# Performance work log

Hardware: AMD Instinct MI355X
Metric: run time of the kernel (lower is better)

## Reference

```python
import jax, jax.numpy as jnp
import numpy as np

MODES = 32
WIDTH = 64


def crelu(z):
    # split-complex ReLU (torch.relu is undefined on complex; this is the standard fix)
    return jax.nn.relu(z.real) + 1j * jax.nn.relu(z.imag)


def _linear_params(key, fan_in, fan_out):
    k1, k2 = jax.random.split(key)
    s = 1.0 / np.sqrt(fan_in)
    W = jax.random.uniform(k1, (fan_out, fan_in), minval=-s, maxval=s, dtype=jnp.float32)
    b = jax.random.uniform(k2, (fan_out,), minval=-s, maxval=s, dtype=jnp.float32)
    return W, b


def setup_inputs() -> dict:
    key = jax.random.key(0)
    ks = jax.random.split(key, 8)
    B, G = 32768, 512
    H0, H1, H2 = 1024, 512, 64  # hidden_layers; H2 == WIDTH
    FD = 128                    # field_dim
    geometry_input = jax.random.normal(ks[0], (B, G), dtype=jnp.float32)
    W_in, b_in = _linear_params(ks[1], G, H0)
    W_h1, b_h1 = _linear_params(ks[2], H0, H1)
    W_h2, b_h2 = _linear_params(ks[3], H1, H2)
    w0 = jax.random.normal(ks[4], (MODES, WIDTH), dtype=jnp.float32)
    w1 = jax.random.normal(ks[5], (MODES, WIDTH), dtype=jnp.float32)
    lin1_W, lin1_b = _linear_params(ks[6], WIDTH, WIDTH)
    k7a, k7b = jax.random.split(ks[7])
    lin2_W, lin2_b = _linear_params(k7a, WIDTH, WIDTH)
    W_out, b_out = _linear_params(k7b, H2, FD)
    return dict(geometry_input=geometry_input, W_in=W_in, b_in=b_in,
                W_h1=W_h1, b_h1=b_h1, W_h2=W_h2, b_h2=b_h2,
                w0=w0, w1=w1, lin1_W=lin1_W, lin1_b=lin1_b,
                lin2_W=lin2_W, lin2_b=lin2_b, W_out=W_out, b_out=b_out)


def reference(geometry_input, W_in, b_in, W_h1, b_h1, W_h2, b_h2,
              w0, w1, lin1_W, lin1_b, lin2_W, lin2_b, W_out, b_out):
    # MLP encoder: [B, G] -> [B, 64]
    x = jax.nn.relu(geometry_input @ W_in.T + b_in)
    x = jax.nn.relu(x @ W_h1.T + b_h1)
    x = jax.nn.relu(x @ W_h2.T + b_h2)
    # FNO block
    xh = jnp.fft.fftn(x)  # fftn over ALL axes, as in torch code -> complex64 [B, 64]
    phase = jnp.exp(1j * 2.0 * jnp.pi * jnp.arange(MODES) / MODES).astype(jnp.complex64)
    y = xh[:, None, :] * w0  # per-mode lift: [B, MODES, WIDTH]
    y = crelu(y)
    y = y * phase[None, :, None]  # diagonal L mode-multiply
    y = jnp.einsum('bmw,mw->bw', y, w1.astype(y.dtype))  # collapse modes -> [B, WIDTH]
    y = crelu(y @ lin1_W.T + lin1_b)  # real weights on complex acts
    y = y @ lin2_W.T + lin2_b
    y = jnp.fft.ifftn(y)  # [B, 64] complex
    out = y @ W_out.T + b_out  # [B, field_dim] complex
    return out
```

## Files before the change

### kernel.cpp

```cpp
#include <hip/hip_runtime.h>
#include <hip/hip_bf16.h>


#define PI2F 6.28318530717958647692f

typedef __attribute__((ext_vector_type(8))) short short8;
typedef __attribute__((ext_vector_type(4))) float f32x4;

__device__ __forceinline__ unsigned short f2bf(float f) {
  unsigned int u = __float_as_uint(f);
  u += 0x7fff + ((u >> 16) & 1);
  return (unsigned short)(u >> 16);
}
__device__ __forceinline__ unsigned int pack_bf16x2(float a, float b) {
  return (unsigned int)f2bf(a) | ((unsigned int)f2bf(b) << 16);
}

__device__ __forceinline__ void gl2lds16(const void* gptr, const void* lptr) {
  __builtin_amdgcn_global_load_lds(
      (const __attribute__((address_space(1))) unsigned int*)(unsigned long long)gptr,
      (__attribute__((address_space(3))) unsigned int*)(unsigned int)(unsigned long long)lptr,
      16, 0, 0);
}

__global__ __launch_bounds__(256) void f32_to_bf16_k(
    const float* __restrict__ src, unsigned short* __restrict__ dst, int n4)
{
  int i = blockIdx.x * 256 + threadIdx.x;
  if (i < n4) {
    float4 v = ((const float4*)src)[i];
    uint2 p;
    p.x = pack_bf16x2(v.x, v.y);
    p.y = pack_bf16x2(v.z, v.w);
    ((uint2*)dst)[i] = p;
  }
}

template<int BM, int BN, int WM, int WN, typename OUT>
__global__ __launch_bounds__(256) void gemm_async(
    const unsigned short* __restrict__ A, const unsigned short* __restrict__ Bw,
    const float* __restrict__ bias, OUT* __restrict__ C,
    int M, int N, int K)
{
  constexpr int BK = 64;
  __shared__ __align__(16) unsigned short lA[BM * BK];
  __shared__ __align__(16) unsigned short lB[BN * BK];
  const int tid = threadIdx.x;
  const int lane = tid & 63;
  const int wv = tid >> 6;
  const int q = lane >> 4, lr = lane & 15;
  const int x7 = lr & 7;
  constexpr int WN_CNT = BN / WN;
  const int wm = (wv / WN_CNT) * WM;
  const int wn = (wv % WN_CNT) * WN;
  const size_t m0 = (size_t)blockIdx.x * BM;
  const size_t n0 = (size_t)blockIdx.y * BN;
  constexpr int MI = WM / 16, NI = WN / 16;
  f32x4 acc[MI][NI] = {};
  constexpr int A_INSTR = BM * BK / 512;
  constexpr int B_INSTR = BN * BK / 512;
  constexpr int A_PW = A_INSTR / 4, B_PW = B_INSTR / 4;
  (void)M;

  for (int k0 = 0; k0 < K; k0 += BK) {
    __syncthreads();
    #pragma unroll
    for (int s = 0; s < A_PW; ++s) {
      int instr = wv * A_PW + s;
      int pc = instr * 64 + lane;
      int row = pc >> 3, col = pc & 7;
      int lc = col ^ (row & 7);
      gl2lds16(A + (m0 + row) * K + k0 + lc * 8, lA + instr * 512);
    }
    #pragma unroll
    for (int s = 0; s < B_PW; ++s) {
      int instr = wv * B_PW + s;
      int pc = instr * 64 + lane;
      int row = pc >> 3, col = pc & 7;
      int lc = col ^ (row & 7);
      gl2lds16(Bw + (n0 + row) * K + k0 + lc * 8, lB + instr * 512);
    }
    __syncthreads();
    #pragma unroll
    for (int t = 0; t < 2; ++t) {
      short8 af[MI], bfr[NI];
      #pragma unroll
      for (int i = 0; i < MI; ++i) {
        int r = wm + i * 16 + lr;
        af[i] = *(const short8*)(lA + r * 64 + (((t << 2) | q) ^ x7) * 8);
      }
      #pragma unroll
      for (int j = 0; j < NI; ++j) {
        int r = wn + j * 16 + lr;
        bfr[j] = *(const short8*)(lB + r * 64 + (((t << 2) | q) ^ x7) * 8);
      }
      #pragma unroll
      for (int i = 0; i < MI; ++i)
        #pragma unroll
        for (int j = 0; j < NI; ++j)
          acc[i][j] = __builtin_amdgcn_mfma_f32_16x16x32_bf16(af[i], bfr[j], acc[i][j], 0, 0, 0);
    }
  }
  #pragma unroll
  for (int i = 0; i < MI; ++i)
    #pragma unroll
    for (int j = 0; j < NI; ++j) {
      size_t col = n0 + wn + j * 16 + lr;
      float bv = bias[col];
      #pragma unroll
      for (int r = 0; r < 4; ++r) {
        size_t row = m0 + wm + i * 16 + q * 4 + r;
        float v = acc[i][j][r] + bv;
        v = v > 0.f ? v : 0.f;
        if (sizeof(OUT) == 2) ((unsigned short*)C)[row * N + col] = f2bf(v);
        else                  ((float*)C)[row * N + col] = v;
      }
    }
}

__global__ __launch_bounds__(256) void precompute(
    const float* __restrict__ w0, const float* __restrict__ w1,
    const float* __restrict__ l2W, const float* __restrict__ l2b,
    float2* __restrict__ Ap, float2* __restrict__ Am,
    float2* __restrict__ Q, float2* __restrict__ b2c)
{
  const int t = threadIdx.x;
  const int blk = blockIdx.x;
  if (blk == 0) {
    if (t < 64) {
      float apx = 0, apy = 0, amx = 0, amy = 0;
      for (int m = 0; m < 32; ++m) {
        float s0 = w0[m * 64 + t];
        float cf = w1[m * 64 + t] * s0;
        float sn, cs; sincosf(PI2F * (float)m / 32.f, &sn, &cs);
        if (s0 > 0.f)      { apx += cs * cf; apy += sn * cf; }
        else if (s0 < 0.f) { amx += cs * cf; amy += sn * cf; }
      }
      Ap[t] = make_float2(apx, apy);
      Am[t] = make_float2(amx, amy);
      float bx = 0, by = 0;
      for (int k = 0; k < 64; ++k) {
        float sn, cs; sincosf(PI2F * (float)((t * k) & 63) / 64.f, &sn, &cs);
        float lb = l2b[k] * (1.f / 64.f);
        bx += cs * lb; by += sn * lb;
      }
      b2c[t] = make_float2(bx, by);
    }
  } else {
    int e = (blk - 1) * 256 + t;
    int j = e >> 6, w = e & 63;
    float qx = 0, qy = 0;
    for (int k = 0; k < 64; ++k) {
      float sn, cs; sincosf(PI2F * (float)((j * k) & 63) / 64.f, &sn, &cs);
      float lw = l2W[k * 64 + w] * (1.f / 64.f);
      qx += cs * lw; qy += sn * lw;
    }
    Q[j * 64 + w] = make_float2(qx, qy);
  }
}

__global__ __launch_bounds__(256) void dft64_rows(
    const float* __restrict__ x3, float2* __restrict__ xh1)
{
  __shared__ float xt[64][64];
  __shared__ float2 tw[64];
  const int t = threadIdx.x;
  const size_t b0 = (size_t)blockIdx.x * 64;
  for (int it = 0; it < 16; ++it) {
    int idx = it * 256 + t;
    int r = idx >> 6, w = idx & 63;
    xt[r][w] = x3[(b0 + r) * 64 + w];
  }
  if (t < 64) {
    float sn, cs; sincosf(-PI2F * (float)t / 64.f, &sn, &cs);
    tw[t] = make_float2(cs, sn);
  }
  __syncthreads();
  const int k = t & 63, rg = t >> 6;
  float2 acc[16] = {};
  #pragma unroll 1
  for (int w = 0; w < 64; ++w) {
    float2 tv = tw[(k * w) & 63];
    #pragma unroll
    for (int r = 0; r < 16; ++r) {
      float xv = xt[rg * 16 + r][w];
      acc[r].x += xv * tv.x;
      acc[r].y += xv * tv.y;
    }
  }
  for (int r = 0; r < 16; ++r)
    xh1[(b0 + rg * 16 + r) * 64 + k] = acc[r];
}

template<int SIGN>
__global__ __launch_bounds__(256) void fft_stage1(
    const float2* __restrict__ Xin, float2* __restrict__ T)
{
  __shared__ float2 tile[128 * 33];
  __shared__ float2 tw16s[16];
  const int blk = blockIdx.x;
  const int b2 = blk >> 1, wh = (blk & 1) * 32;
  const int t = threadIdx.x;
  for (int it = 0; it < 16; ++it) {
    int idx = it * 256 + t;
    int b1 = idx >> 5, wi = idx & 31;
    tile[b1 * 33 + wi] = Xin[((size_t)(b1 * 256 + b2)) * 64 + wh + wi];
  }
  if (t < 16) {
    float sn, cs; sincosf(SIGN * PI2F * (float)t / 16.f, &sn, &cs);
    tw16s[t] = make_float2(cs, sn);
  }
  __syncthreads();
  const int p = t >> 1, n2a = p >> 4, k1pa = p & 15, w0 = (t & 1) * 16;
  float2 ya[16] = {};
  #pragma unroll 1
  for (int n1 = 0; n1 < 16; ++n1) {
    float2 tv = tw16s[(n1 * k1pa) & 15];
    const float2* row = &tile[(8 * n1 + n2a) * 33 + w0];
    #pragma unroll
    for (int w = 0; w < 16; ++w) {
      float2 d = row[w];
      ya[w].x += d.x * tv.x - d.y * tv.y;
      ya[w].y += d.x * tv.y + d.y * tv.x;
    }
  }
  {
    float sn, cs; sincosf(SIGN * PI2F * (float)(n2a * k1pa) / 128.f, &sn, &cs);
    #pragma unroll
    for (int w = 0; w < 16; ++w) {
      float2 a = ya[w];
      ya[w] = make_float2(a.x * cs - a.y * sn, a.x * sn + a.y * cs);
    }
  }
  __syncthreads();
  {
    float2* yrow = &tile[(n2a * 16 + k1pa) * 33 + w0];
    #pragma unroll
    for (int w = 0; w < 16; ++w) yrow[w] = ya[w];
  }
  __syncthreads();
  const int wB = t & 31, qB = t >> 5;
  float sstep, cstep;
  sincosf(SIGN * PI2F * (float)(16 * b2) / 32768.f, &sstep, &cstep);
  #pragma unroll 1
  for (int h = 0; h < 2; ++h) {
    const int k1p = qB + 8 * h;
    float2 acc[8] = {};
    #pragma unroll 1
    for (int n2 = 0; n2 < 8; ++n2) {
      float2 d = tile[(n2 * 16 + k1p) * 33 + wB];
      #pragma unroll
      for (int k2p = 0; k2p < 8; ++k2p) {
        float2 tv = tw16s[(2 * n2 * k2p) & 15];
        acc[k2p].x += d.x * tv.x - d.y * tv.y;
        acc[k2p].y += d.x * tv.y + d.y * tv.x;
      }
    }
    float sb, cb;
    sincosf(SIGN * PI2F * (float)(b2 * k1p) / 32768.f, &sb, &cb);
    float2 rot = make_float2(cb, sb);
    #pragma unroll
    for (int k2p = 0; k2p < 8; ++k2p) {
      int k1 = k1p + 16 * k2p;
      float2 a = acc[k2p];
      float2 o = make_float2(a.x * rot.x - a.y * rot.y,
                             a.x * rot.y + a.y * rot.x);
      T[((size_t)k1 * 256 + b2) * 64 + wh + wB] = o;
      float nrx = rot.x * cstep - rot.y * sstep;
      rot.y = rot.x * sstep + rot.y * cstep;
      rot.x = nrx;
    }
  }
}

template<int SIGN, bool SCALE>
__global__ __launch_bounds__(256) void fft_stage2(
    const float2* __restrict__ T, float2* __restrict__ X)
{
  __shared__ float2 tile[256 * 17];
  __shared__ float2 tw16s[16];
  const int blk = blockIdx.x;
  const int k1 = blk >> 2, wq = (blk & 3) * 16;
  const int t = threadIdx.x;
  for (int it = 0; it < 16; ++it) {
    int idx = it * 256 + t;
    int r2 = idx >> 4, wi = idx & 15;
    tile[r2 * 17 + wi] = T[((size_t)k1 * 256 + r2) * 64 + wq + wi];
  }
  if (t < 16) {
    float sn, cs; sincosf(SIGN * PI2F * (float)t / 16.f, &sn, &cs);
    tw16s[t] = make_float2(cs, sn);
  }
  __syncthreads();
  const int n2a = t >> 4, k1pa = t & 15;
  float2 ya[16] = {};
  #pragma unroll 1
  for (int n1 = 0; n1 < 16; ++n1) {
    float2 tv = tw16s[(n1 * k1pa) & 15];
    const float2* row = &tile[(16 * n1 + n2a) * 17];
    #pragma unroll
    for (int w = 0; w < 16; ++w) {
      float2 d = row[w];
      ya[w].x += d.x * tv.x - d.y * tv.y;
      ya[w].y += d.x * tv.y + d.y * tv.x;
    }
  }
  {
    float sn, cs; sincosf(SIGN * PI2F * (float)(n2a * k1pa) / 256.f, &sn, &cs);
    #pragma unroll
    for (int w = 0; w < 16; ++w) {
      float2 a = ya[w];
      ya[w] = make_float2(a.x * cs - a.y * sn, a.x * sn + a.y * cs);
    }
  }
  __syncthreads();
  {
    float2* yrow = &tile[(n2a * 16 + k1pa) * 17];
    #pragma unroll
    for (int w = 0; w < 16; ++w) yrow[w] = ya[w];
  }
  __syncthreads();
  const int k1pb = t >> 4, wB = t & 15;
  float2 acc[16] = {};
  #pragma unroll 1
  for (int n2 = 0; n2 < 16; ++n2) {
    float2 d = tile[(n2 * 16 + k1pb) * 17 + wB];
    #pragma unroll
    for (int k2p = 0; k2p < 16; ++k2p) {
      float2 tv = tw16s[(n2 * k2p) & 15];
      acc[k2p].x += d.x * tv.x - d.y * tv.y;
      acc[k2p].y += d.x * tv.y + d.y * tv.x;
    }
  }
  const float sc = SCALE ? (1.f / 32768.f) : 1.f;
  #pragma unroll
  for (int k2p = 0; k2p < 16; ++k2p) {
    int k2 = k1pb + 16 * k2p;
    size_t row = (size_t)(k1 + 128 * k2);
    X[row * 64 + wq + wB] = make_float2(acc[k2p].x * sc, acc[k2p].y * sc);
  }
}

__global__ __launch_bounds__(256) void pw_lin(
    const float2* __restrict__ xh,
    const float2* __restrict__ Ap, const float2* __restrict__ Am,
    const float* __restrict__ l1W, const float* __restrict__ l1b,
    const float2* __restrict__ Q, const float2* __restrict__ b2c,
    float2* __restrict__ u)
{
  __shared__ float2 yt[32][64];
  __shared__ float2 zt[32][64];
  const int t = threadIdx.x;
  const size_t b0 = (size_t)blockIdx.x * 32;
  for (int it = 0; it < 8; ++it) {
    int idx = it * 256 + t;
    int r = idx >> 6, w = idx & 63;
    float2 xv = xh[(b0 + r) * 64 + w];
    float2 Aa = (xv.x >= 0.f) ? Ap[w] : Am[w];
    float2 Ab = (xv.y >= 0.f) ? Ap[w] : Am[w];
    float c1r = xv.x * Aa.x, c1i = xv.x * Aa.y;
    float c2r = xv.y * Ab.x, c2i = xv.y * Ab.y;
    yt[r][w] = make_float2(c1r - c2i, c1i + c2r);
  }
  __syncthreads();
  {
    const int n = t & 63, rg = t >> 6;
    float2 acc[8] = {};
    #pragma unroll 1
    for (int w = 0; w < 64; ++w) {
      float lw = l1W[n * 64 + w];
      #pragma unroll
      for (int r = 0; r < 8; ++r) {
        float2 yv = yt[rg * 8 + r][w];
        acc[r].x += yv.x * lw;
        acc[r].y += yv.y * lw;
      }
    }
    float bb = l1b[n];
    #pragma unroll
    for (int r = 0; r < 8; ++r) {
      float zr = acc[r].x + bb; zr = zr > 0.f ? zr : 0.f;
      float zi = acc[r].y;      zi = zi > 0.f ? zi : 0.f;
      zt[rg * 8 + r][n] = make_float2(zr, zi);
    }
  }
  __syncthreads();
  {
    const int j = t & 63, rg = t >> 6;
    float2 acc[8] = {};
    #pragma unroll 1
    for (int w = 0; w < 64; ++w) {
      float2 qv = Q[j * 64 + w];
      #pragma unroll
      for (int r = 0; r < 8; ++r) {
        float2 zv = zt[rg * 8 + r][w];
        acc[r].x += zv.x * qv.x - zv.y * qv.y;
        acc[r].y += zv.x * qv.y + zv.y * qv.x;
      }
    }
    float2 bc = b2c[j];
    #pragma unroll
    for (int r = 0; r < 8; ++r)
      u[(b0 + rg * 8 + r) * 64 + j] = make_float2(acc[r].x + bc.x, acc[r].y + bc.y);
  }
}

template<int MODE>
__global__ __launch_bounds__(256) void final_out(
    const float2* __restrict__ v, const float* __restrict__ Wout,
    const float* __restrict__ bout, float* __restrict__ out)
{
  __shared__ float2 vt[64][64];
  const int t = threadIdx.x;
  const size_t b0 = (size_t)blockIdx.x * 64;
  for (int it = 0; it < 16; ++it) {
    int idx = it * 256 + t;
    int r = idx >> 6, w = idx & 63;
    vt[r][w] = v[(b0 + r) * 64 + w];
  }
  __syncthreads();
  const int f = t & 127, rg = t >> 7;
  float2 acc[32] = {};
  #pragma unroll 1
  for (int j = 0; j < 64; ++j) {
    float wv = Wout[f * 64 + j];
    #pragma unroll
    for (int r = 0; r < 32; ++r) {
      float2 vv = vt[rg * 32 + r][j];
      acc[r].x += vv.x * wv;
      acc[r].y += vv.y * wv;
    }
  }
  float bb = bout[f];
  #pragma unroll
  for (int r = 0; r < 32; ++r) {
    size_t idx = (b0 + rg * 32 + r) * 128 + f;
    if (MODE == 0) out[idx] = acc[r].x + bb;
    else ((float2*)out)[idx] = make_float2(acc[r].x + bb, acc[r].y);
  }
}

extern "C" void kernel_launch(void* const* d_in, const int* in_sizes, int n_in,
                              void* d_out, int out_size, void* d_ws, size_t ws_size,
                              hipStream_t stream)
{
  (void)in_sizes; (void)n_in; (void)ws_size;
  const float* geom = (const float*)d_in[0];
  const float* Win  = (const float*)d_in[1];
  const float* bin  = (const float*)d_in[2];
  const float* Wh1  = (const float*)d_in[3];
  const float* bh1  = (const float*)d_in[4];
  const float* Wh2  = (const float*)d_in[5];
  const float* bh2  = (const float*)d_in[6];
  const float* w0   = (const float*)d_in[7];
  const float* w1   = (const float*)d_in[8];
  const float* l1W  = (const float*)d_in[9];
  const float* l1b  = (const float*)d_in[10];
  const float* l2W  = (const float*)d_in[11];
  const float* l2b  = (const float*)d_in[12];
  const float* Wout = (const float*)d_in[13];
  const float* bout = (const float*)d_in[14];

  char* ws = (char*)d_ws;
  const size_t MB = 1048576ull;
  unsigned short* geomb = (unsigned short*)(ws);
  unsigned short* x2b   = (unsigned short*)(ws);
  unsigned short* x1b   = (unsigned short*)(ws + 32 * MB);
  float*  x3  = (float*)(ws + 32 * MB);
  float2* S0  = (float2*)(ws + 40 * MB);
  float2* S1  = (float2*)(ws + 56 * MB);
  float2* Ap  = (float2*)(ws + 72 * MB);
  float2* Am  = (float2*)(ws + 72 * MB + 512);
  float2* b2c = (float2*)(ws + 72 * MB + 1024);
  float2* Q   = (float2*)(ws + 72 * MB + 1536);
  unsigned short* Winb = (unsigned short*)(ws + 96 * MB);
  unsigned short* Wh1b = (unsigned short*)(ws + 97 * MB);
  unsigned short* Wh2b = (unsigned short*)(ws + 98 * MB);

  f32_to_bf16_k<<<16384, 256, 0, stream>>>(geom, geomb, 4194304);
  f32_to_bf16_k<<<512, 256, 0, stream>>>(Win, Winb, 131072);
  f32_to_bf16_k<<<512, 256, 0, stream>>>(Wh1, Wh1b, 131072);
  f32_to_bf16_k<<<32, 256, 0, stream>>>(Wh2, Wh2b, 8192);

  gemm_async<128,128,64,64,unsigned short><<<dim3(256, 8), 256, 0, stream>>>(
      geomb, Winb, bin, x1b, 32768, 1024, 512);
  gemm_async<128,128,64,64,unsigned short><<<dim3(256, 4), 256, 0, stream>>>(
      x1b, Wh1b, bh1, x2b, 32768, 512, 1024);
  gemm_async<128, 64,64,32,float><<<dim3(256, 1), 256, 0, stream>>>(
      x2b, Wh2b, bh2, x3, 32768, 64, 512);

  precompute<<<17, 256, 0, stream>>>(w0, w1, l2W, l2b, Ap, Am, Q, b2c);
  dft64_rows<<<512, 256, 0, stream>>>(x3, S0);
  fft_stage1<-1><<<512, 256, 0, stream>>>(S0, S1);
  fft_stage2<-1, false><<<512, 256, 0, stream>>>(S1, S0);
  pw_lin<<<1024, 256, 0, stream>>>(S0, Ap, Am, l1W, l1b, Q, b2c, S1);
  fft_stage1<1><<<512, 256, 0, stream>>>(S1, S0);
  fft_stage2<1, true><<<512, 256, 0, stream>>>(S0, S1);
  if (out_size >= 8388608) {
    final_out<1><<<512, 256, 0, stream>>>(S1, Wout, bout, (float*)d_out);
  } else {
    final_out<0><<<512, 256, 0, stream>>>(S1, Wout, bout, (float*)d_out);
  }
}
```

Baseline: 478.6 us.

## Vectorize LDS reads in DFT, pointwise and output kernels; stage transposed Q in LDS

The row DFT and the final output kernel now handle 32 rows per block instead of 64, with twice as many blocks. Their inner loops read activations from LDS as float4 and unroll the reduction by four. pw_lin receives Q pre-transposed from precompute and copies it into LDS with direct global-to-LDS loads. It also reuses one LDS tile for both stages and drops the middle barrier, since each wave reads only its own rows. The aim is fewer LDS and global load instructions and better occupancy, at the cost of depending on wave-local ordering and on the async Q copy completing before the block barrier.

```diff
diff --git a/kernel.cpp b/kernel.cpp
--- a/kernel.cpp
+++ b/kernel.cpp
@@ -122,7 +122,7 @@
     const float* __restrict__ w0, const float* __restrict__ w1,
     const float* __restrict__ l2W, const float* __restrict__ l2b,
     float2* __restrict__ Ap, float2* __restrict__ Am,
-    float2* __restrict__ Q, float2* __restrict__ b2c)
+    float2* __restrict__ Qt, float2* __restrict__ b2c)
 {
   const int t = threadIdx.x;
   const int blk = blockIdx.x;
@@ -155,18 +155,18 @@
       float lw = l2W[k * 64 + w] * (1.f / 64.f);
       qx += cs * lw; qy += sn * lw;
     }
-    Q[j * 64 + w] = make_float2(qx, qy);
+    Qt[w * 64 + j] = make_float2(qx, qy);
   }
 }
 
 __global__ __launch_bounds__(256) void dft64_rows(
     const float* __restrict__ x3, float2* __restrict__ xh1)
 {
-  __shared__ float xt[64][64];
+  __shared__ __align__(16) float xt[32][64];
   __shared__ float2 tw[64];
   const int t = threadIdx.x;
-  const size_t b0 = (size_t)blockIdx.x * 64;
-  for (int it = 0; it < 16; ++it) {
+  const size_t b0 = (size_t)blockIdx.x * 32;
+  for (int it = 0; it < 8; ++it) {
     int idx = it * 256 + t;
     int r = idx >> 6, w = idx & 63;
     xt[r][w] = x3[(b0 + r) * 64 + w];
@@ -177,19 +177,25 @@
   }
   __syncthreads();
   const int k = t & 63, rg = t >> 6;
-  float2 acc[16] = {};
+  float2 acc[8] = {};
   #pragma unroll 1
-  for (int w = 0; w < 64; ++w) {
-    float2 tv = tw[(k * w) & 63];
-    #pragma unroll
-    for (int r = 0; r < 16; ++r) {
-      float xv = xt[rg * 16 + r][w];
-      acc[r].x += xv * tv.x;
-      acc[r].y += xv * tv.y;
-    }
-  }
-  for (int r = 0; r < 16; ++r)
-    xh1[(b0 + rg * 16 + r) * 64 + k] = acc[r];
+  for (int w4 = 0; w4 < 16; ++w4) {
+    int w = 4 * w4;
+    int kw = k * w;
+    float2 t0 = tw[kw & 63];
+    float2 t1 = tw[(kw + k) & 63];
+    float2 t2 = tw[(kw + 2 * k) & 63];
+    float2 t3 = tw[(kw + 3 * k) & 63];
+    #pragma unroll
+    for (int r = 0; r < 8; ++r) {
+      float4 xv = *(const float4*)(&xt[rg * 8 + r][w]);
+      acc[r].x += xv.x * t0.x + xv.y * t1.x + xv.z * t2.x + xv.w * t3.x;
+      acc[r].y += xv.x * t0.y + xv.y * t1.y + xv.z * t2.y + xv.w * t3.y;
+    }
+  }
+  #pragma unroll
+  for (int r = 0; r < 8; ++r)
+    xh1[(b0 + rg * 8 + r) * 64 + k] = acc[r];
 }
 
 template<int SIGN>
@@ -345,35 +351,52 @@
     const float2* __restrict__ xh,
     const float2* __restrict__ Ap, const float2* __restrict__ Am,
     const float* __restrict__ l1W, const float* __restrict__ l1b,
-    const float2* __restrict__ Q, const float2* __restrict__ b2c,
+    const float2* __restrict__ Qt, const float2* __restrict__ b2c,
     float2* __restrict__ u)
 {
-  __shared__ float2 yt[32][64];
-  __shared__ float2 zt[32][64];
+  __shared__ __align__(16) float2 tile[32][64];
+  __shared__ __align__(16) float2 qt[64 * 64];
   const int t = threadIdx.x;
+  const int lane = t & 63;
+  const int wv = t >> 6;
   const size_t b0 = (size_t)blockIdx.x * 32;
+
+  #pragma unroll
+  for (int s = 0; s < 8; ++s) {
+    int instr = wv * 8 + s;
+    gl2lds16((const char*)Qt + instr * 1024 + lane * 16,
+             (const char*)qt + instr * 1024);
+  }
+
   for (int it = 0; it < 8; ++it) {
     int idx = it * 256 + t;
     int r = idx >> 6, w = idx & 63;
     float2 xv = xh[(b0 + r) * 64 + w];
     float2 Aa = (xv.x >= 0.f) ? Ap[w] : Am[w];
     float2 Ab = (xv.y >= 0.f) ? Ap[w] : Am[w];
-    float c1r = xv.x * Aa.x, c1i = xv.x * Aa.y;
-    float c2r = xv.y * Ab.x, c2i = xv.y * Ab.y;
-    yt[r][w] = make_float2(c1r - c2i, c1i + c2r);
-  }
-  __syncthreads();
+    tile[r][w] = make_float2(xv.x * Aa.x - xv.y * Ab.y,
+                             xv.x * Aa.y + xv.y * Ab.x);
+  }
+  __syncthreads();
+
+  const int n = lane, rg = wv;
+
   {
-    const int n = t & 63, rg = t >> 6;
     float2 acc[8] = {};
+    const float* wrow = l1W + n * 64;
+    float4 lwn = *(const float4*)wrow;
     #pragma unroll 1
-    for (int w = 0; w < 64; ++w) {
-      float lw = l1W[n * 64 + w];
+    for (int w2 = 0; w2 < 16; ++w2) {
+      float4 lw = lwn;
+      lwn = *(const float4*)(wrow + 4 * ((w2 + 1) & 15));
+      int w = 4 * w2;
       #pragma unroll
       for (int r = 0; r < 8; ++r) {
-        float2 yv = yt[rg * 8 + r][w];
-        acc[r].x += yv.x * lw;
-        acc[r].y += yv.y * lw;
+        const float4* rowp = (const float4*)(&tile[rg * 8 + r][w]);
+        float4 y01 = rowp[0];
+        float4 y23 = rowp[1];
+        acc[r].x += y01.x * lw.x + y01.z * lw.y + y23.x * lw.z + y23.z * lw.w;
+        acc[r].y += y01.y * lw.x + y01.w * lw.y + y23.y * lw.z + y23.w * lw.w;
       }
     }
     float bb = l1b[n];
@@ -381,21 +404,33 @@
     for (int r = 0; r < 8; ++r) {
       float zr = acc[r].x + bb; zr = zr > 0.f ? zr : 0.f;
       float zi = acc[r].y;      zi = zi > 0.f ? zi : 0.f;
-      zt[rg * 8 + r][n] = make_float2(zr, zi);
-    }
-  }
-  __syncthreads();
+      tile[rg * 8 + r][n] = make_float2(zr, zi);
+    }
+  }
+
   {
-    const int j = t & 63, rg = t >> 6;
+    const int j = lane;
     float2 acc[8] = {};
     #pragma unroll 1
-    for (int w = 0; w < 64; ++w) {
-      float2 qv = Q[j * 64 + w];
+    for (int w2 = 0; w2 < 16; ++w2) {
+      int w = 4 * w2;
+      float2 q0 = qt[(w + 0) * 64 + j];
+      float2 q1 = qt[(w + 1) * 64 + j];
+      float2 q2 = qt[(w + 2) * 64 + j];
+      float2 q3 = qt[(w + 3) * 64 + j];
       #pragma unroll
       for (int r = 0; r < 8; ++r) {
-        float2 zv = zt[rg * 8 + r][w];
-        acc[r].x += zv.x * qv.x - zv.y * qv.y;
-        acc[r].y += zv.x * qv.y + zv.y * qv.x;
+        const float4* rowp = (const float4*)(&tile[rg * 8 + r][w]);
+        float4 z01 = rowp[0];
+        float4 z23 = rowp[1];
+        acc[r].x += z01.x * q0.x - z01.y * q0.y
+                  + z01.z * q1.x - z01.w * q1.y
+                  + z23.x * q2.x - z23.y * q2.y
+                  + z23.z * q3.x - z23.w * q3.y;
+        acc[r].y += z01.x * q0.y + z01.y * q0.x
+                  + z01.z * q1.y + z01.w * q1.x
+                  + z23.x * q2.y + z23.y * q2.x
+                  + z23.z * q3.y + z23.w * q3.x;
       }
     }
     float2 bc = b2c[j];
@@ -410,31 +445,34 @@
     const float2* __restrict__ v, const float* __restrict__ Wout,
     const float* __restrict__ bout, float* __restrict__ out)
 {
-  __shared__ float2 vt[64][64];
+  __shared__ __align__(16) float2 vt[32][64];
   const int t = threadIdx.x;
-  const size_t b0 = (size_t)blockIdx.x * 64;
-  for (int it = 0; it < 16; ++it) {
+  const size_t b0 = (size_t)blockIdx.x * 32;
+  for (int it = 0; it < 8; ++it) {
     int idx = it * 256 + t;
     int r = idx >> 6, w = idx & 63;
     vt[r][w] = v[(b0 + r) * 64 + w];
   }
   __syncthreads();
   const int f = t & 127, rg = t >> 7;
-  float2 acc[32] = {};
+  const float* wrow = Wout + f * 64;
+  float2 acc[16] = {};
+  float2 wvn = *(const float2*)wrow;
   #pragma unroll 1
-  for (int j = 0; j < 64; ++j) {
-    float wv = Wout[f * 64 + j];
-    #pragma unroll
-    for (int r = 0; r < 32; ++r) {
-      float2 vv = vt[rg * 32 + r][j];
-      acc[r].x += vv.x * wv;
-      acc[r].y += vv.y * wv;
+  for (int j2 = 0; j2 < 32; ++j2) {
+    float2 wc = wvn;
+    wvn = *(const float2*)(wrow + 2 * ((j2 + 1) & 31));
+    #pragma unroll
+    for (int r = 0; r < 16; ++r) {
+      float4 vv = *(const float4*)(&vt[rg * 16 + r][2 * j2]);
+      acc[r].x += vv.x * wc.x + vv.z * wc.y;
+      acc[r].y += vv.y * wc.x + vv.w * wc.y;
     }
   }
   float bb = bout[f];
   #pragma unroll
-  for (int r = 0; r < 32; ++r) {
-    size_t idx = (b0 + rg * 32 + r) * 128 + f;
+  for (int r = 0; r < 16; ++r) {
+    size_t idx = (b0 + rg * 16 + r) * 128 + f;
     if (MODE == 0) out[idx] = acc[r].x + bb;
     else ((float2*)out)[idx] = make_float2(acc[r].x + bb, acc[r].y);
   }
@@ -472,7 +510,7 @@
   float2* Ap  = (float2*)(ws + 72 * MB);
   float2* Am  = (float2*)(ws + 72 * MB + 512);
   float2* b2c = (float2*)(ws + 72 * MB + 1024);
-  float2* Q   = (float2*)(ws + 72 * MB + 1536);
+  float2* Qt  = (float2*)(ws + 72 * MB + 1536);
   unsigned short* Winb = (unsigned short*)(ws + 96 * MB);
   unsigned short* Wh1b = (unsigned short*)(ws + 97 * MB);
   unsigned short* Wh2b = (unsigned short*)(ws + 98 * MB);
@@ -489,16 +527,16 @@
   gemm_async<128, 64,64,32,float><<<dim3(256, 1), 256, 0, stream>>>(
       x2b, Wh2b, bh2, x3, 32768, 64, 512);
 
-  precompute<<<17, 256, 0, stream>>>(w0, w1, l2W, l2b, Ap, Am, Q, b2c);
-  dft64_rows<<<512, 256, 0, stream>>>(x3, S0);
+  precompute<<<17, 256, 0, stream>>>(w0, w1, l2W, l2b, Ap, Am, Qt, b2c);
+  dft64_rows<<<1024, 256, 0, stream>>>(x3, S0);
   fft_stage1<-1><<<512, 256, 0, stream>>>(S0, S1);
   fft_stage2<-1, false><<<512, 256, 0, stream>>>(S1, S0);
-  pw_lin<<<1024, 256, 0, stream>>>(S0, Ap, Am, l1W, l1b, Q, b2c, S1);
+  pw_lin<<<1024, 256, 0, stream>>>(S0, Ap, Am, l1W, l1b, Qt, b2c, S1);
   fft_stage1<1><<<512, 256, 0, stream>>>(S1, S0);
   fft_stage2<1, true><<<512, 256, 0, stream>>>(S0, S1);
   if (out_size >= 8388608) {
-    final_out<1><<<512, 256, 0, stream>>>(S1, Wout, bout, (float*)d_out);
+    final_out<1><<<1024, 256, 0, stream>>>(S1, Wout, bout, (float*)d_out);
   } else {
-    final_out<0><<<512, 256, 0, stream>>>(S1, Wout, bout, (float*)d_out);
-  }
-}
+    final_out<0><<<1024, 256, 0, stream>>>(S1, Wout, bout, (float*)d_out);
+  }
+}
```

Result: faster. 450.2 us (-5.9%).
